# Optimization experiments

Hardware: AMD Instinct MI355X
Metric: run time of the kernel (lower is better)

The kernel has to match this reference:

```python
import jax, jax.numpy as jnp
import numpy as np
from jax import lax

# ---- model dims (match init_kwargs) ----
D = 2048        # hidden_size
HD = 128        # head_dim
HQ = 16         # num_q_heads (= expanded_num_heads)
HK = 8          # num_k_heads = num_v_heads
CONV = 4        # conv_size
CHUNK = 64      # chunk_size
NUM_ITER = 30   # chebyshev iterations
RIDGE = 0.02
EPS = 1e-6


def setup_inputs() -> dict:
    key = jax.random.key(0)
    ks = jax.random.split(key, 20)
    s = 0.02
    inp = {}
    inp['hidden_states'] = jax.random.normal(ks[0], (1, 1024, D), jnp.float32)
    inp['Wq'] = jax.random.normal(ks[1], (D, HQ * HD), jnp.float32) * s
    inp['Wk'] = jax.random.normal(ks[2], (D, HK * HD), jnp.float32) * s
    inp['Wv'] = jax.random.normal(ks[3], (D, HK * HD), jnp.float32) * s
    inp['conv_q'] = jax.random.normal(ks[4], (HQ * HD, CONV), jnp.float32) * 0.3
    inp['conv_k'] = jax.random.normal(ks[5], (HK * HD, CONV), jnp.float32) * 0.3
    inp['conv_v'] = jax.random.normal(ks[6], (HK * HD, CONV), jnp.float32) * 0.3
    inp['Wa'] = jax.random.normal(ks[7], (D, HQ), jnp.float32) * s
    # A_log = log(Uniform(0,16)) as in torch init
    inp['A_log'] = jnp.log(jax.random.uniform(ks[8], (HQ,), jnp.float32, 1e-3, 16.0))
    # dt_bias = inverse-softplus of dt ~ LogUniform(1e-3, 1e-1)
    dt = jnp.exp(jax.random.uniform(ks[9], (HQ,), jnp.float32) * (np.log(0.1) - np.log(0.001)) + np.log(0.001))
    dt = jnp.clip(dt, 1e-4, None)
    inp['dt_bias'] = dt + jnp.log(-jnp.expm1(-dt))
    inp['Wb'] = jax.random.normal(ks[10], (D, HQ), jnp.float32) * s
    inp['bb'] = jnp.zeros((HQ,), jnp.float32)
    inp['Walpha'] = jax.random.normal(ks[11], (D, HQ), jnp.float32) * s
    inp['balpha'] = jnp.zeros((HQ,), jnp.float32)
    inp['Wg'] = jax.random.normal(ks[12], (D, HQ * HD), jnp.float32) * s
    inp['norm_w'] = jnp.ones((HD,), jnp.float32)
    inp['Wo'] = jax.random.normal(ks[13], (HQ * HD, D), jnp.float32) * s
    return inp


def short_conv(x, w):
    # causal depthwise conv1d (kernel=CONV) + silu; x:[B,L,C], w:[C,K]
    K = w.shape[1]
    L = x.shape[1]
    xp = jnp.pad(x, ((0, 0), (K - 1, 0), (0, 0)))
    y = sum(xp[:, j:j + L, :] * w[:, j] for j in range(K))
    return jax.nn.silu(y)


def cheb_solve(A, b, lmin, lmax, num_iter):
    # Chebyshev semi-iteration for SPD A x = b, eigenvalue bounds [lmin, lmax].
    # A, b: [..., d, d]; lmin scalar; lmax: [..., 1, 1]
    theta = (lmax + lmin) / 2.0
    delta = (lmax - lmin) / 2.0
    sigma1 = theta / delta
    x = jnp.zeros_like(b)
    r = b
    rho = 1.0 / sigma1
    dvec = r / theta
    def body(carry, _):
        x, r, dvec, rho = carry
        x = x + dvec
        r = r - jnp.einsum('...de,...ef->...df', A, dvec)
        rho_n = 1.0 / (2.0 * sigma1 - rho)
        dvec = rho_n * rho * dvec + (2.0 * rho_n / delta) * r
        return (x, r, dvec, rho_n), None
    (x, _, _, _), _ = lax.scan(body, (x, r, dvec, rho), None, length=num_iter)
    return x


def reference(hidden_states, Wq, Wk, Wv, conv_q, conv_k, conv_v, Wa, A_log, dt_bias,
              Wb, bb, Walpha, balpha, Wg, norm_w, Wo):
    x = hidden_states
    B, L, _ = x.shape
    H, Hk, d, C = HQ, HK, HD, CHUNK
    Nc = L // C

    # projections + short causal convs with silu
    q = short_conv(x @ Wq, conv_q).reshape(B, L, H, d) * (d ** -0.5)  # gla rescale
    k = short_conv(x @ Wk, conv_k).reshape(B, L, Hk, d)
    v = short_conv(x @ Wv, conv_v).reshape(B, L, Hk, d)
    grp = H // Hk
    k = jnp.repeat(k, grp, axis=2)  # GQA expand: (h g) ordering
    v = jnp.repeat(v, grp, axis=2)

    # gates
    glog = -jnp.exp(A_log) * jax.nn.softplus(x @ Wa + dt_bias)   # [B,L,H], log forgetting gate <= 0
    beta = jax.nn.sigmoid(x @ Wb + bb)                           # [B,L,H]
    alpha = jax.nn.sigmoid(x @ Walpha + balpha)                  # [B,L,H]

    # chunk: [B,H,Nc,C,...]
    def ch(t):
        return t.reshape(B, Nc, C, H, -1).transpose(0, 3, 1, 2, 4)
    qc, kc, vc = ch(q), ch(k), ch(v)
    glc = glog.reshape(B, Nc, C, H).transpose(0, 3, 1, 2)   # [B,H,Nc,C]
    bc = beta.reshape(B, Nc, C, H).transpose(0, 3, 1, 2)

    cs = jnp.cumsum(glc, axis=-1)         # inclusive cumulative log-decay within chunk
    G = cs[..., -1]                        # total chunk decay [B,H,Nc]
    w_end = jnp.exp(G[..., None] - cs) * bc
    dHn = jnp.einsum('bhnc,bhncd,bhnce->bhnde', w_end, kc, kc)  # gram increment (forgetting_gate_kk)
    dBn = jnp.einsum('bhnc,bhncd,bhnce->bhnde', w_end, kc, vc)  # kv increment
    dg = jnp.exp(G)

    # inter-chunk state recurrence (scan over chunks)
    def step(carry, inp):
        Hs, Bs = carry
        g_n, dH_n, dB_n = inp
        out = (Hs, Bs)  # state at chunk START
        Hs = g_n[..., None, None] * Hs + dH_n
        Bs = g_n[..., None, None] * Bs + dB_n
        return (Hs, Bs), out
    init = (jnp.zeros((B, H, d, d), x.dtype), jnp.zeros((B, H, d, d), x.dtype))
    inputs = (dg.transpose(2, 0, 1), dHn.transpose(2, 0, 1, 3, 4), dBn.transpose(2, 0, 1, 3, 4))
    _, (H0, B0) = lax.scan(step, init, inputs)  # [Nc,B,H,d,d]

    # ridge-regularized Kalman solve per chunk via Chebyshev
    A = H0 + RIDGE * jnp.eye(d, dtype=x.dtype)
    lmax = jnp.trace(A, axis1=-2, axis2=-1)[..., None, None]  # trace >= lambda_max for SPD
    X = cheb_solve(A, B0, RIDGE, lmax, NUM_ITER)              # [Nc,B,H,d,d]
    Xc = X.transpose(1, 2, 0, 3, 4)                           # [B,H,Nc,d,d]

    # inter-chunk readout (through solved state)
    o_inter = jnp.exp(cs)[..., None] * jnp.einsum('bhncd,bhnde->bhnce', qc, Xc)
    # intra-chunk causal gated attention
    diff = cs[..., :, None] - cs[..., None, :]                # [B,H,Nc,C,C]
    mask = jnp.tril(jnp.ones((C, C), bool))
    dmat = jnp.exp(jnp.where(mask, diff, -1e30))
    scores = jnp.einsum('bhncd,bhnjd->bhncj', qc, kc) * dmat * bc[..., None, :]
    o_intra = jnp.einsum('bhncj,bhnjd->bhncd', scores, vc)

    o = (o_inter + o_intra).transpose(0, 2, 3, 1, 4).reshape(B, L, H, d)
    o = o + alpha[..., None] * v   # alpha connection (residual value path)

    # gated RMSNorm + output projection
    g_out = (x @ Wg).reshape(B, L, H, d)
    o = o * lax.rsqrt(jnp.mean(o * o, axis=-1, keepdims=True) + EPS) * norm_w
    o = o * jax.nn.silu(g_out)
    return o.reshape(B, L, H * d) @ Wo
```

## Files before the change

### kernel.cpp

```cpp
#include <hip/hip_runtime.h>
#include <math.h>


#define LSEQ 1024
#define DM   2048
#define NHQ  16
#define NHK  8
#define HDIM 128
#define NCH  16
#define CSZ  64

typedef __attribute__((ext_vector_type(8))) short short8;
typedef __attribute__((ext_vector_type(4))) float floatx4;

__device__ __forceinline__ unsigned short f2bf(float f) {
  unsigned int u = __float_as_uint(f);
  u += 0x7fffu + ((u >> 16) & 1u);
  return (unsigned short)(u >> 16);
}
__device__ __forceinline__ float bf2f(unsigned short u) {
  return __uint_as_float(((unsigned int)u) << 16);
}

__device__ __forceinline__ void tcast_fat(
    const float* __restrict__ W, unsigned short* __restrict__ Wt,
    int K, int N, int bn, int bk, int tid, float* __restrict__ t) {
  int k0 = bk * 128, n0 = bn * 64;
#pragma unroll
  for (int i = 0; i < 8; ++i) {
    int u = tid + i * 256;
    int r = u >> 4, c4 = u & 15;
    float4 v = *(const float4*)(W + (size_t)(k0 + r) * N + n0 + c4 * 4);
    float* dst = t + r * 65 + c4 * 4;
    dst[0] = v.x; dst[1] = v.y; dst[2] = v.z; dst[3] = v.w;
  }
  __syncthreads();
#pragma unroll
  for (int i = 0; i < 4; ++i) {
    int u2 = tid + i * 256;
    int klow = u2 & 7, nlow = (u2 >> 3) & 7;
    int khigh = (u2 >> 6) & 1, nhigh = (u2 >> 7) & 7;
    int k8 = (klow + khigh * 8) * 8;
    int nn = nlow + nhigh * 8;
    unsigned short o8[8];
#pragma unroll
    for (int j = 0; j < 8; ++j) o8[j] = f2bf(t[(k8 + j) * 65 + nn]);
    *(uint4*)(Wt + (size_t)(n0 + nn) * K + k0 + k8) = *(uint4*)o8;
  }
}

__global__ __launch_bounds__(256) void prep_kernel(
    const float* __restrict__ x, const float* __restrict__ Wq,
    const float* __restrict__ Wk, const float* __restrict__ Wv,
    const float* __restrict__ Wg, unsigned short* __restrict__ xb16,
    unsigned short* __restrict__ WtAll,
    const float* __restrict__ Wa, const float* __restrict__ Wbeta,
    const float* __restrict__ Wal, const float* __restrict__ A_log,
    const float* __restrict__ dtb, const float* __restrict__ bbv,
    const float* __restrict__ balv, float* __restrict__ glog,
    float* __restrict__ beta, float* __restrict__ alpha) {
  __shared__ float smem[128 * 65];
  int b = blockIdx.x, tid = threadIdx.x;
  if (b < 1024) {
    float* xr = smem;
    float* part = smem + 2048;
    int ts = b;
    for (int i = tid; i < 512; i += 256)
      ((float4*)xr)[i] = ((const float4*)(x + (size_t)ts * 2048))[i];
    __syncthreads();
    int o = tid >> 2, p = tid & 3;
    float s = 0.f;
    if (o < 48) {
      const float* W = (o < 16) ? Wa : (o < 32) ? Wbeta : Wal;
      int h = o & 15;
      int k0 = p * 512;
      for (int k = k0; k < k0 + 512; ++k) s = fmaf(xr[k], W[k * 16 + h], s);
    }
    part[tid] = s;
    __syncthreads();
    if (o < 48 && p == 0) {
      float dot = part[tid] + part[tid + 1] + part[tid + 2] + part[tid + 3];
      int h = o & 15;
      if (o < 16) {
        float za = dot + dtb[h];
        float sp = fmaxf(za, 0.f) + log1pf(expf(-fabsf(za)));
        glog[ts * 16 + h] = -expf(A_log[h]) * sp;
      } else if (o < 32) {
        beta[ts * 16 + h] = 1.f / (1.f + expf(-(dot + bbv[h])));
      } else {
        alpha[ts * 16 + h] = 1.f / (1.f + expf(-(dot + balv[h])));
      }
    }
  } else if (b < 2560) {
    int r = b - 1024;
    if (r < 512) {
      tcast_fat(Wq, WtAll, 2048, 2048, r & 31, r >> 5, tid, smem);
    } else if (r < 768) {
      int q = r - 512;
      tcast_fat(Wk, WtAll + (size_t)2048 * 2048, 2048, 1024, q & 15, q >> 4,
                tid, smem);
    } else if (r < 1024) {
      int q = r - 768;
      tcast_fat(Wv, WtAll + (size_t)3072 * 2048, 2048, 1024, q & 15, q >> 4,
                tid, smem);
    } else {
      int q = r - 1024;
      tcast_fat(Wg, WtAll + (size_t)4096 * 2048, 2048, 2048, q & 31, q >> 5,
                tid, smem);
    }
  } else {
    int i0 = (b - 2560) * 1024 + tid;
#pragma unroll
    for (int i = 0; i < 4; ++i) {
      int idx = i0 + i * 256;
      float4 v = ((const float4*)x)[idx];
      ushort4 u;
      u.x = f2bf(v.x); u.y = f2bf(v.y); u.z = f2bf(v.z); u.w = f2bf(v.w);
      ((ushort4*)xb16)[idx] = u;
    }
  }
}

__global__ __launch_bounds__(256) void gemm_bf16(
    const unsigned short* __restrict__ A, const unsigned short* __restrict__ Bt,
    float* __restrict__ C, int M, int N, int K) {
  __shared__ unsigned short As[128 * 72];
  __shared__ unsigned short Bs[64 * 72];
  int tid = threadIdx.x;
  int wave = tid >> 6, lane = tid & 63;
  int ln = lane & 15, hi = lane >> 4;
  int wm = wave & 1, wn = wave >> 1;
  int m0 = blockIdx.y * 128, n0 = blockIdx.x * 64;

  floatx4 acc[4][2];
#pragma unroll
  for (int mt = 0; mt < 4; ++mt)
#pragma unroll
    for (int nt = 0; nt < 2; ++nt) acc[mt][nt] = (floatx4)(0.f);

  for (int k0 = 0; k0 < K; k0 += 64) {
#pragma unroll
    for (int g = 0; g < 4; ++g) {
      int l = tid + g * 256;
      int m = l >> 3, go = l & 7;
      uint4 v = *(const uint4*)(A + (size_t)(m0 + m) * K + k0 + go * 8);
      *(uint4*)(As + m * 72 + go * 8) = v;
    }
#pragma unroll
    for (int g = 0; g < 2; ++g) {
      int l = tid + g * 256;
      int n = l >> 3, go = l & 7;
      uint4 v = *(const uint4*)(Bt + (size_t)(n0 + n) * K + k0 + go * 8);
      *(uint4*)(Bs + n * 72 + go * 8) = v;
    }
    __syncthreads();
#pragma unroll
    for (int kb = 0; kb < 2; ++kb) {
      short8 a[4], b[2];
#pragma unroll
      for (int mt = 0; mt < 4; ++mt)
        a[mt] = *(const short8*)(As + (wm * 64 + mt * 16 + ln) * 72 + kb * 32 + hi * 8);
#pragma unroll
      for (int nt = 0; nt < 2; ++nt)
        b[nt] = *(const short8*)(Bs + (wn * 32 + nt * 16 + ln) * 72 + kb * 32 + hi * 8);
#pragma unroll
      for (int mt = 0; mt < 4; ++mt)
#pragma unroll
        for (int nt = 0; nt < 2; ++nt)
          acc[mt][nt] = __builtin_amdgcn_mfma_f32_16x16x32_bf16(
              a[mt], b[nt], acc[mt][nt], 0, 0, 0);
    }
    __syncthreads();
  }
#pragma unroll
  for (int mt = 0; mt < 4; ++mt)
#pragma unroll
    for (int nt = 0; nt < 2; ++nt) {
      int col = n0 + wn * 32 + nt * 16 + ln;
      int rowb = m0 + wm * 64 + mt * 16 + hi * 4;
#pragma unroll
      for (int r = 0; r < 4; ++r)
        C[(size_t)(rowb + r) * N + col] = acc[mt][nt][r];
    }
}

__device__ __forceinline__ float conv_core(
    const float* __restrict__ xin, const float* __restrict__ w,
    int idx, int instride, int nch, float scale) {
  int t = idx / nch, ch = idx - t * nch;
  float acc = 0.f;
#pragma unroll
  for (int j = 0; j < 4; ++j) {
    int tt = t + j - 3;
    float xv = (tt >= 0) ? xin[(size_t)tt * instride + ch] : 0.f;
    acc = fmaf(xv, w[ch * 4 + j], acc);
  }
  return acc / (1.f + expf(-acc)) * scale;
}

__global__ __launch_bounds__(256) void conv_all(
    const float* __restrict__ xall, const float* __restrict__ convq,
    const float* __restrict__ convk, const float* __restrict__ convv,
    unsigned short* __restrict__ qs16, float* __restrict__ ks2,
    unsigned short* __restrict__ ks16, float* __restrict__ vs2,
    const float* __restrict__ glog, const float* __restrict__ beta,
    float* __restrict__ cs, float* __restrict__ wend) {
  int b = blockIdx.x, tid = threadIdx.x;
  if (b < 8192) {
    int idx = b * 256 + tid;
    qs16[idx] = f2bf(conv_core(xall, convq, idx, 6144, 2048,
                               0.08838834764831845f));
  } else if (b < 12288) {
    int idx = (b - 8192) * 256 + tid;
    float v = conv_core(xall + 2048, convk, idx, 6144, 1024, 1.0f);
    ks2[idx] = v;
    ks16[idx] = f2bf(v);
  } else if (b < 16384) {
    int idx = (b - 12288) * 256 + tid;
    vs2[idx] = conv_core(xall + 3072, convv, idx, 6144, 1024, 1.0f);
  } else {
    int idx = tid;
    int n = idx & 15;
    float acc = 0.f;
    for (int c = 0; c < CSZ; ++c) {
      acc += glog[(n * CSZ + c) * NHQ + (idx >> 4)];
      cs[idx * CSZ + c] = acc;
    }
    float G = acc;
    for (int c = 0; c < CSZ; ++c) {
      wend[idx * CSZ + c] =
          expf(G - cs[idx * CSZ + c]) * beta[(n * CSZ + c) * NHQ + (idx >> 4)];
    }
  }
}

__global__ __launch_bounds__(256) void dhb_kernel(
    const float* __restrict__ ks, const float* __restrict__ vs,
    const float* __restrict__ wend, float* __restrict__ dH,
    float* __restrict__ dB, unsigned short* __restrict__ vT16) {
  __shared__ uint4 smem4[4096];
  int bid = blockIdx.x;
  int tid = threadIdx.x;

  if (bid >= 256) {
    float* t = (float*)smem4;
    int b = bid - 256;
    size_t gbase = ((size_t)(b >> 3)) * 65536 + ((size_t)(b & 7)) * 128;
#pragma unroll
    for (int g = 0; g < 8; ++g) {
      int i = tid + g * 256;
      int c = i >> 5, e4 = i & 31;
      float4 v = *(const float4*)(vs + gbase + (size_t)c * 1024 + e4 * 4);
      t[c * 132 + e4 * 4 + 0] = v.x;
      t[c * 132 + e4 * 4 + 1] = v.y;
      t[c * 132 + e4 * 4 + 2] = v.z;
      t[c * 132 + e4 * 4 + 3] = v.w;
    }
    __syncthreads();
    int e = tid >> 1, half = tid & 1;
    size_t obase = ((size_t)b << 13) + (size_t)e * 64 + half * 32;
#pragma unroll
    for (int cc = 0; cc < 8; ++cc) {
      int c0 = half * 32 + cc * 4;
      ushort4 u;
      u.x = f2bf(t[(c0 + 0) * 132 + e]);
      u.y = f2bf(t[(c0 + 1) * 132 + e]);
      u.z = f2bf(t[(c0 + 2) * 132 + e]);
      u.w = f2bf(t[(c0 + 3) * 132 + e]);
      *(ushort4*)(vT16 + obase + cc * 4) = u;
    }
    return;
  }

  unsigned short (*skF)[8192] = (unsigned short (*)[8192])smem4;
  unsigned short (*svF)[8192] =
      (unsigned short (*)[8192])((unsigned short*)smem4 + 16384);
  int h = bid >> 4, n = bid & 15;
  int hk = h >> 1;

#pragma unroll
  for (int p = 0; p < 4; ++p) {
    int t2 = tid + p * 256;
    int c0 = (t2 >> 7) << 3;
    int e = t2 & 127;
    int base = ((e >> 4) * 2 + (c0 >> 5)) * 512 +
               ((c0 & 31) >> 3) * 128 + (e & 15) * 8;
    unsigned short kh[8], kl[8], vh[8], vl[8];
#pragma unroll
    for (int j = 0; j < 8; ++j) {
      int c = c0 + j;
      float s = sqrtf(wend[bid * 64 + c]);
      size_t g = (size_t)(n * 64 + c) * 1024 + hk * 128 + e;
      float kf = s * ks[g];
      float vf = s * vs[g];
      unsigned short khh = f2bf(kf);
      kh[j] = khh; kl[j] = f2bf(kf - bf2f(khh));
      unsigned short vhh = f2bf(vf);
      vh[j] = vhh; vl[j] = f2bf(vf - bf2f(vhh));
    }
    *(uint4*)(&skF[0][base]) = *(uint4*)kh;
    *(uint4*)(&skF[1][base]) = *(uint4*)kl;
    *(uint4*)(&svF[0][base]) = *(uint4*)vh;
    *(uint4*)(&svF[1][base]) = *(uint4*)vl;
  }
  __syncthreads();

  int w = tid >> 6, lane = tid & 63;
  int ln = lane & 15, hi = lane >> 4;

  short8 ah[2][2], al[2][2];
#pragma unroll
  for (int mti = 0; mti < 2; ++mti) {
    int mt = w * 2 + mti;
#pragma unroll
    for (int ct = 0; ct < 2; ++ct) {
      ah[mti][ct] = *(const short8*)(&skF[0][((mt * 2 + ct) * 64 + lane) * 8]);
      al[mti][ct] = *(const short8*)(&skF[1][((mt * 2 + ct) * 64 + lane) * 8]);
    }
  }

  size_t gb = (size_t)bid << 14;
#pragma unroll
  for (int which = 0; which < 2; ++which) {
    const unsigned short (*BF)[8192] = which ? svF : skF;
    float* outp = which ? dB : dH;
#pragma unroll
    for (int nt = 0; nt < 8; ++nt) {
      floatx4 a0 = (floatx4)(0.f), a1 = (floatx4)(0.f);
#pragma unroll
      for (int ct = 0; ct < 2; ++ct) {
        short8 bh = *(const short8*)(&BF[0][((nt * 2 + ct) * 64 + lane) * 8]);
        short8 bl = *(const short8*)(&BF[1][((nt * 2 + ct) * 64 + lane) * 8]);
        a0 = __builtin_amdgcn_mfma_f32_16x16x32_bf16(ah[0][ct], bh, a0, 0, 0, 0);
        a0 = __builtin_amdgcn_mfma_f32_16x16x32_bf16(ah[0][ct], bl, a0, 0, 0, 0);
        a0 = __builtin_amdgcn_mfma_f32_16x16x32_bf16(al[0][ct], bh, a0, 0, 0, 0);
        a1 = __builtin_amdgcn_mfma_f32_16x16x32_bf16(ah[1][ct], bh, a1, 0, 0, 0);
        a1 = __builtin_amdgcn_mfma_f32_16x16x32_bf16(ah[1][ct], bl, a1, 0, 0, 0);
        a1 = __builtin_amdgcn_mfma_f32_16x16x32_bf16(al[1][ct], bh, a1, 0, 0, 0);
      }
      int e = nt * 16 + ln;
#pragma unroll
      for (int rg = 0; rg < 4; ++rg) {
        int d0 = (w * 2 + 0) * 16 + hi * 4 + rg;
        int d1 = (w * 2 + 1) * 16 + hi * 4 + rg;
        outp[gb + (size_t)d0 * 128 + e] = a0[rg];
        outp[gb + (size_t)d1 * 128 + e] = a1[rg];
      }
    }
  }
}

__global__ __launch_bounds__(256) void scan_kernel(
    float* __restrict__ dH, float* __restrict__ dB,
    const float* __restrict__ cs) {
  int idx = blockIdx.x * 256 + threadIdx.x;
  int h = idx >> 14, de = idx & 16383;
  float Hs = 0.f, Bs = 0.f;
  bool diag = ((de % 129) == 0);
#pragma unroll 1
  for (int n = 0; n < NCH; ++n) {
    size_t off = ((size_t)(h * 16 + n) << 14) + de;
    float dh = dH[off], db = dB[off];
    dH[off] = diag ? (Hs + 0.02f) : Hs;
    dB[off] = Bs;
    float g = expf(cs[(h * 16 + n) * CSZ + (CSZ - 1)]);
    Hs = fmaf(g, Hs, dh);
    Bs = fmaf(g, Bs, db);
  }
}

__global__ __launch_bounds__(256) void afrag_kernel(
    float* __restrict__ Aall, float* __restrict__ traces) {
  int bid = blockIdx.x;
  float* Ag = Aall + ((size_t)bid << 14);
  __shared__ float As[16384];
  int tid = threadIdx.x;
  for (int i = tid; i < 4096; i += 256)
    ((float4*)As)[i] = ((const float4*)Ag)[i];
  __syncthreads();
  if (tid < 64) {
    float tv = As[tid * 129] + As[(tid + 64) * 129];
#pragma unroll
    for (int off = 32; off; off >>= 1) tv += __shfl_down(tv, off);
    if (tid == 0) traces[bid] = tv;
  }
  unsigned short* Ah = (unsigned short*)Ag;
  unsigned short* Al = Ah + 16384;
#pragma unroll
  for (int c8 = 0; c8 < 8; ++c8) {
    int s0 = tid * 64 + c8 * 8;
    int frag = s0 >> 9, mlane = (s0 >> 3) & 63;
    int m = ((frag >> 2) << 4) + (mlane & 15);
    int k = ((frag & 3) << 5) + ((mlane >> 4) << 3);
    unsigned short hi[8], lo[8];
#pragma unroll
    for (int j = 0; j < 8; ++j) {
      float a = As[m * 128 + k + j];
      unsigned short h = f2bf(a);
      hi[j] = h;
      lo[j] = f2bf(a - bf2f(h));
    }
    *(uint4*)(Ah + s0) = *(uint4*)hi;
    *(uint4*)(Al + s0) = *(uint4*)lo;
  }
}

__global__ __launch_bounds__(256, 4) void cheb_kernel(
    const unsigned short* __restrict__ Afrag, const float* __restrict__ traces,
    float* __restrict__ Ball) {
  int bid = blockIdx.x;
  int bm = bid & 255;
  int cb = bid >> 8;
  const unsigned short* __restrict__ Ah = Afrag + ((size_t)bm << 15);
  float* __restrict__ Bg = Ball + ((size_t)bm << 14);
  __shared__ unsigned short dT[2][2048];
  int tid = threadIdx.x;
  int w = tid >> 6, lane = tid & 63;
  int ln = lane & 15, q = lane >> 4;

  float lmax = traces[bm];
  const float lmin = 0.02f;
  float theta = 0.5f * (lmax + lmin);
  float delta = 0.5f * (lmax - lmin);
  float sigma1 = theta / delta;
  float rho = delta / theta;
  float invtheta = 1.f / theta;

  short8 afr[2][4][2];
#pragma unroll
  for (int mt = 0; mt < 2; ++mt)
#pragma unroll
    for (int kt = 0; kt < 4; ++kt) {
      int f = (w * 2 + mt) * 4 + kt;
      afr[mt][kt][0] = *(const short8*)(Ah + ((f * 64 + lane) << 3));
      afr[mt][kt][1] = *(const short8*)(Ah + 16384 + ((f * 64 + lane) << 3));
    }

  int wrB[2];
#pragma unroll
  for (int mt = 0; mt < 2; ++mt)
    wrB[mt] = w * 512 + (((mt * 2 + (q >> 1)) & 3) * 16 + ln) * 8 +
              ((q & 1) << 2);

  float xx[2][4], rr[2][4], dd[2][4];
#pragma unroll
  for (int mt = 0; mt < 2; ++mt) {
    ushort4 pack;
    unsigned short* pp = (unsigned short*)&pack;
#pragma unroll
    for (int rg = 0; rg < 4; ++rg) {
      float b = Bg[(w * 32 + mt * 16 + q * 4 + rg) * 128 + cb * 16 + ln];
      rr[mt][rg] = b;
      xx[mt][rg] = 0.f;
      unsigned short dq = f2bf(b * invtheta);
      dd[mt][rg] = bf2f(dq);
      pp[rg] = dq;
    }
    *(ushort4*)(&dT[0][wrB[mt]]) = pack;
  }
  __syncthreads();

#pragma unroll 1
  for (int it = 0; it < 30; ++it) {
    const unsigned short* dTr = dT[it & 1];
    unsigned short* dTw = dT[(it & 1) ^ 1];
    floatx4 a0 = (floatx4)(0.f), a1 = (floatx4)(0.f);
#pragma unroll
    for (int kt = 0; kt < 4; ++kt) {
      short8 df = *(const short8*)(dTr + kt * 512 + lane * 8);
      a0 = __builtin_amdgcn_mfma_f32_16x16x32_bf16(afr[0][kt][0], df, a0, 0, 0, 0);
      a0 = __builtin_amdgcn_mfma_f32_16x16x32_bf16(afr[0][kt][1], df, a0, 0, 0, 0);
      a1 = __builtin_amdgcn_mfma_f32_16x16x32_bf16(afr[1][kt][0], df, a1, 0, 0, 0);
      a1 = __builtin_amdgcn_mfma_f32_16x16x32_bf16(afr[1][kt][1], df, a1, 0, 0, 0);
    }
    float rho_n = 1.f / (2.f * sigma1 - rho);
    float c1s = rho_n * rho;
    float c2s = 2.f * rho_n / delta;
#pragma unroll
    for (int mt = 0; mt < 2; ++mt) {
      ushort4 pack;
      unsigned short* pp = (unsigned short*)&pack;
#pragma unroll
      for (int rg = 0; rg < 4; ++rg) {
        xx[mt][rg] += dd[mt][rg];
        rr[mt][rg] -= mt ? a1[rg] : a0[rg];
        float dn = fmaf(c1s, dd[mt][rg], c2s * rr[mt][rg]);
        unsigned short dq = f2bf(dn);
        dd[mt][rg] = bf2f(dq);
        pp[rg] = dq;
      }
      *(ushort4*)(&dTw[wrB[mt]]) = pack;
    }
    rho = rho_n;
    __syncthreads();
  }

  unsigned short* Xf = (unsigned short*)Bg;
#pragma unroll
  for (int mt = 0; mt < 2; ++mt) {
    ushort4 h4, l4;
    unsigned short* hp = (unsigned short*)&h4;
    unsigned short* lp = (unsigned short*)&l4;
#pragma unroll
    for (int rg = 0; rg < 4; ++rg) {
      float xv = xx[mt][rg];
      unsigned short h = f2bf(xv);
      hp[rg] = h;
      lp[rg] = f2bf(xv - bf2f(h));
    }
    int lhi = wrB[mt];
    int llo = lhi + 2048;
    *(ushort4*)(Xf + ((lhi >> 5) << 8) + (cb << 5) + (lhi & 31)) = h4;
    *(ushort4*)(Xf + ((llo >> 5) << 8) + (cb << 5) + (llo & 31)) = l4;
  }
}

__global__ __launch_bounds__(256) void attn_kernel(
    const unsigned short* __restrict__ q16, const unsigned short* __restrict__ k16,
    const unsigned short* __restrict__ vT16, const unsigned short* __restrict__ Xf,
    const float* __restrict__ vs, const float* __restrict__ cs,
    const float* __restrict__ beta, const float* __restrict__ alpha,
    float* __restrict__ o) {
  int bid = blockIdx.x;
  int h = bid >> 4, n = bid & 15;
  int hk = h >> 1;
  __shared__ unsigned short qb[64 * 136];
  __shared__ unsigned short kb[64 * 136];
  __shared__ unsigned short Sb[64 * 72];
  __shared__ float csL[64], ecsL[64], betaL[64], alphaL[64];
  int tid = threadIdx.x;
  int w = tid >> 6, lane = tid & 63;
  int ln = lane & 15, hi = lane >> 4;

  {
    size_t qgb = (((size_t)(n * 64)) * 16 + h) * 128;
    size_t kgb = (((size_t)(n * 64)) * 8 + hk) * 128;
#pragma unroll
    for (int g = 0; g < 4; ++g) {
      int i = tid + g * 256;
      int c = i >> 4, ch = i & 15;
      *(uint4*)(qb + c * 136 + ch * 8) =
          *(const uint4*)(q16 + qgb + (size_t)c * 2048 + ch * 8);
      *(uint4*)(kb + c * 136 + ch * 8) =
          *(const uint4*)(k16 + kgb + (size_t)c * 1024 + ch * 8);
    }
    if (tid < 64) {
      float cv = cs[bid * 64 + tid];
      csL[tid] = cv;
      ecsL[tid] = expf(cv);
      betaL[tid] = beta[(n * 64 + tid) * 16 + h];
      alphaL[tid] = alpha[(n * 64 + tid) * 16 + h];
    }
  }
  __syncthreads();

  short8 aq[4];
#pragma unroll
  for (int dt = 0; dt < 4; ++dt)
    aq[dt] = *(const short8*)(qb + (w * 16 + ln) * 136 + dt * 32 + hi * 8);

  const unsigned short* Xb = Xf + ((size_t)bid << 15);
  floatx4 acc[8];
#pragma unroll
  for (int et = 0; et < 8; ++et) {
    floatx4 a = (floatx4)(0.f);
#pragma unroll
    for (int dt = 0; dt < 4; ++dt) {
      int base = ((dt * 16 + (lane >> 2)) << 8) + (et << 5) + ((lane & 3) << 3);
      short8 xh = *(const short8*)(Xb + base);
      short8 xl = *(const short8*)(Xb + base + 16384);
      a = __builtin_amdgcn_mfma_f32_16x16x32_bf16(aq[dt], xh, a, 0, 0, 0);
      a = __builtin_amdgcn_mfma_f32_16x16x32_bf16(aq[dt], xl, a, 0, 0, 0);
    }
    acc[et] = a;
  }
#pragma unroll
  for (int et = 0; et < 8; ++et)
#pragma unroll
    for (int rg = 0; rg < 4; ++rg)
      acc[et][rg] *= ecsL[w * 16 + hi * 4 + rg];

#pragma unroll
  for (int jt = 0; jt < 4; ++jt) {
    if (jt <= w) {
      floatx4 s = (floatx4)(0.f);
#pragma unroll
      for (int dt = 0; dt < 4; ++dt) {
        short8 bk = *(const short8*)(kb + (jt * 16 + ln) * 136 + dt * 32 + hi * 8);
        s = __builtin_amdgcn_mfma_f32_16x16x32_bf16(aq[dt], bk, s, 0, 0, 0);
      }
      int j = jt * 16 + ln;
      float csj = csL[j], bj = betaL[j];
#pragma unroll
      for (int rg = 0; rg < 4; ++rg) {
        int c = w * 16 + hi * 4 + rg;
        float v = (j <= c) ? s[rg] * expf(csL[c] - csj) * bj : 0.f;
        Sb[c * 72 + j] = f2bf(v);
      }
    } else {
#pragma unroll
      for (int rg = 0; rg < 4; ++rg)
        Sb[(w * 16 + hi * 4 + rg) * 72 + jt * 16 + ln] = 0;
    }
  }

  const unsigned short* vTb = vT16 + ((size_t)(n * 8 + hk) << 13);
#pragma unroll
  for (int et = 0; et < 8; ++et) {
#pragma unroll
    for (int kt = 0; kt < 2; ++kt) {
      short8 as = *(const short8*)(Sb + (w * 16 + ln) * 72 + kt * 32 + hi * 8);
      short8 bv = *(const short8*)(vTb + (et * 16 + ln) * 64 + kt * 32 + hi * 8);
      acc[et] = __builtin_amdgcn_mfma_f32_16x16x32_bf16(as, bv, acc[et], 0, 0, 0);
    }
  }

#pragma unroll
  for (int et = 0; et < 8; ++et) {
#pragma unroll
    for (int rg = 0; rg < 4; ++rg) {
      int c = w * 16 + hi * 4 + rg, e = et * 16 + ln;
      size_t oaddr = (((size_t)(n * 64 + c)) * 16 + h) * 128 + e;
      size_t vaddr = (((size_t)(n * 64 + c)) * 8 + hk) * 128 + e;
      o[oaddr] = acc[et][rg] + alphaL[c] * vs[vaddr];
    }
  }
}

__global__ __launch_bounds__(256) void rmso_kernel(
    const float* __restrict__ o, const float* __restrict__ xall,
    const float* __restrict__ norm_w, unsigned short* __restrict__ onorm,
    const float* __restrict__ Wo, unsigned short* __restrict__ WtWo) {
  __shared__ float t[128 * 65];
  int b = blockIdx.x, tid = threadIdx.x;
  if (b < 512) {
    tcast_fat(Wo, WtWo, 2048, 2048, b & 31, b >> 5, tid, t);
  } else {
    int bb = b - 512;
    int wave = tid >> 6, lane = tid & 63;
    int row = bb * 4 + wave;
    size_t base = (size_t)row * HDIM;
    size_t gbase = (size_t)(row >> 4) * 6144 + 4096 + (size_t)(row & 15) * HDIM;
    float v0 = o[base + lane], v1 = o[base + lane + 64];
    float ss = fmaf(v0, v0, v1 * v1);
#pragma unroll
    for (int off = 32; off; off >>= 1) ss += __shfl_down(ss, off);
    ss = __shfl(ss, 0);
    float rinv = rsqrtf(ss * (1.f / 128.f) + 1e-6f);
    float g0 = xall[gbase + lane], g1 = xall[gbase + lane + 64];
    float s0 = g0 / (1.f + expf(-g0));
    float s1 = g1 / (1.f + expf(-g1));
    onorm[base + lane]      = f2bf(v0 * rinv * norm_w[lane] * s0);
    onorm[base + lane + 64] = f2bf(v1 * rinv * norm_w[lane + 64] * s1);
  }
}

extern "C" void kernel_launch(void* const* d_in, const int* in_sizes, int n_in,
                              void* d_out, int out_size, void* d_ws,
                              size_t ws_size, hipStream_t stream) {
  (void)in_sizes; (void)n_in; (void)out_size; (void)ws_size;
  const float* x      = (const float*)d_in[0];
  const float* Wq     = (const float*)d_in[1];
  const float* Wk     = (const float*)d_in[2];
  const float* Wv     = (const float*)d_in[3];
  const float* convq  = (const float*)d_in[4];
  const float* convk  = (const float*)d_in[5];
  const float* convv  = (const float*)d_in[6];
  const float* Wa     = (const float*)d_in[7];
  const float* A_log  = (const float*)d_in[8];
  const float* dtb    = (const float*)d_in[9];
  const float* Wb     = (const float*)d_in[10];
  const float* bbv    = (const float*)d_in[11];
  const float* Wal    = (const float*)d_in[12];
  const float* balv   = (const float*)d_in[13];
  const float* Wg     = (const float*)d_in[14];
  const float* norm_w = (const float*)d_in[15];
  const float* Wo     = (const float*)d_in[16];
  float* out = (float*)d_out;

  float* p = (float*)d_ws;
  float* xall  = p; p += 6291456;
  float* qslot = p; p += 2097152;
  float* ks2   = p; p += 1048576;
  float* vs2   = p; p += 1048576;
  float* ob    = p; p += 2097152;
  float* glog  = p; p += 16384;
  float* beta  = p; p += 16384;
  float* alpha = p; p += 16384;
  float* csb   = p; p += 16384;
  float* wend  = p; p += 16384;
  float* traces= p; p += 16384;
  float* dHn   = p; p += 4194304;
  float* dBn   = p; p += 4194304;
  unsigned short* xb16 = (unsigned short*)p; p += 1048576;

  unsigned short* qs16 = (unsigned short*)qslot;
  unsigned short* ks16 = qs16 + 2097152;
  unsigned short* vT16 = ks16 + 1048576;
  unsigned short* WtAll = (unsigned short*)dHn;
  unsigned short* WtWo  = (unsigned short*)ks2;
  unsigned short* onorm16 = xb16;

  dim3 blk(256);
  prep_kernel<<<3072, blk, 0, stream>>>(x, Wq, Wk, Wv, Wg, xb16, WtAll,
                                        Wa, Wb, Wal, A_log, dtb, bbv, balv,
                                        glog, beta, alpha);
  gemm_bf16<<<dim3(96, 8), blk, 0, stream>>>(xb16, WtAll, xall, 1024, 6144, 2048);
  conv_all<<<16385, blk, 0, stream>>>(xall, convq, convk, convv,
                                      qs16, ks2, ks16, vs2,
                                      glog, beta, csb, wend);
  dhb_kernel<<<384, blk, 0, stream>>>(ks2, vs2, wend, dHn, dBn, vT16);
  scan_kernel<<<1024, blk, 0, stream>>>(dHn, dBn, csb);
  afrag_kernel<<<256, blk, 0, stream>>>(dHn, traces);
  cheb_kernel<<<2048, blk, 0, stream>>>((unsigned short*)dHn, traces, dBn);
  attn_kernel<<<256, blk, 0, stream>>>(qs16, ks16, vT16, (unsigned short*)dBn,
                                       vs2, csb, beta, alpha, ob);
  rmso_kernel<<<4608, blk, 0, stream>>>(ob, xall, norm_w, onorm16, Wo, WtWo);
  gemm_bf16<<<dim3(32, 8), blk, 0, stream>>>(onorm16, WtWo, out, 1024, 2048, 2048);
}
```

Baseline: 420.4 us.

## Use direct global-to-LDS loads and wider N tile in bf16 GEMM

Replaces register-staged global loads with global_load_lds direct-to-LDS transfers in the GEMM and templatizes the N tile width, using 128 columns for the QKVG projection. This aims to cut VGPR traffic and instruction count in tile loading and to improve reuse of A tiles. LDS padding is removed, because direct loads need contiguous rows, which risks LDS bank conflicts on the fragment reads.

```diff
diff --git a/kernel.cpp b/kernel.cpp
--- a/kernel.cpp
+++ b/kernel.cpp
@@ -20,6 +20,13 @@
 }
 __device__ __forceinline__ float bf2f(unsigned short u) {
   return __uint_as_float(((unsigned int)u) << 16);
+}
+
+__device__ __forceinline__ void gload16(const unsigned short* g,
+                                        unsigned short* l) {
+  __builtin_amdgcn_global_load_lds(
+      (const __attribute__((address_space(1))) unsigned int*)g,
+      (__attribute__((address_space(3))) unsigned int*)l, 16, 0, 0);
 }
 
 __device__ __forceinline__ void tcast_fat(
@@ -121,52 +128,54 @@
   }
 }
 
-__global__ __launch_bounds__(256) void gemm_bf16(
+template <int BN>
+__global__ __launch_bounds__(256) void gemm_lds(
     const unsigned short* __restrict__ A, const unsigned short* __restrict__ Bt,
     float* __restrict__ C, int M, int N, int K) {
-  __shared__ unsigned short As[128 * 72];
-  __shared__ unsigned short Bs[64 * 72];
+  __shared__ unsigned short As[128 * 64];
+  __shared__ unsigned short Bs[BN * 64];
+  constexpr int NT = BN / 32;
+  constexpr int BCH = BN / 32;
   int tid = threadIdx.x;
   int wave = tid >> 6, lane = tid & 63;
   int ln = lane & 15, hi = lane >> 4;
   int wm = wave & 1, wn = wave >> 1;
-  int m0 = blockIdx.y * 128, n0 = blockIdx.x * 64;
-
-  floatx4 acc[4][2];
+  int m0 = blockIdx.y * 128, n0 = blockIdx.x * BN;
+  int lrow = lane >> 3, lcol = (lane & 7) * 8;
+
+  floatx4 acc[4][NT];
 #pragma unroll
   for (int mt = 0; mt < 4; ++mt)
 #pragma unroll
-    for (int nt = 0; nt < 2; ++nt) acc[mt][nt] = (floatx4)(0.f);
+    for (int nt = 0; nt < NT; ++nt) acc[mt][nt] = (floatx4)(0.f);
 
   for (int k0 = 0; k0 < K; k0 += 64) {
 #pragma unroll
-    for (int g = 0; g < 4; ++g) {
-      int l = tid + g * 256;
-      int m = l >> 3, go = l & 7;
-      uint4 v = *(const uint4*)(A + (size_t)(m0 + m) * K + k0 + go * 8);
-      *(uint4*)(As + m * 72 + go * 8) = v;
-    }
-#pragma unroll
-    for (int g = 0; g < 2; ++g) {
-      int l = tid + g * 256;
-      int n = l >> 3, go = l & 7;
-      uint4 v = *(const uint4*)(Bt + (size_t)(n0 + n) * K + k0 + go * 8);
-      *(uint4*)(Bs + n * 72 + go * 8) = v;
+    for (int i = 0; i < 4; ++i) {
+      int c = wave * 4 + i;
+      gload16(A + (size_t)(m0 + c * 8 + lrow) * K + k0 + lcol, As + c * 512);
+    }
+#pragma unroll
+    for (int i = 0; i < BCH; ++i) {
+      int c = wave * BCH + i;
+      gload16(Bt + (size_t)(n0 + c * 8 + lrow) * K + k0 + lcol, Bs + c * 512);
     }
     __syncthreads();
 #pragma unroll
     for (int kb = 0; kb < 2; ++kb) {
-      short8 a[4], b[2];
+      short8 a[4], b[NT];
 #pragma unroll
       for (int mt = 0; mt < 4; ++mt)
-        a[mt] = *(const short8*)(As + (wm * 64 + mt * 16 + ln) * 72 + kb * 32 + hi * 8);
-#pragma unroll
-      for (int nt = 0; nt < 2; ++nt)
-        b[nt] = *(const short8*)(Bs + (wn * 32 + nt * 16 + ln) * 72 + kb * 32 + hi * 8);
+        a[mt] = *(const short8*)(As + (wm * 64 + mt * 16 + ln) * 64 +
+                                 kb * 32 + hi * 8);
+#pragma unroll
+      for (int nt = 0; nt < NT; ++nt)
+        b[nt] = *(const short8*)(Bs + (wn * (BN / 2) + nt * 16 + ln) * 64 +
+                                 kb * 32 + hi * 8);
 #pragma unroll
       for (int mt = 0; mt < 4; ++mt)
 #pragma unroll
-        for (int nt = 0; nt < 2; ++nt)
+        for (int nt = 0; nt < NT; ++nt)
           acc[mt][nt] = __builtin_amdgcn_mfma_f32_16x16x32_bf16(
               a[mt], b[nt], acc[mt][nt], 0, 0, 0);
     }
@@ -175,8 +184,8 @@
 #pragma unroll
   for (int mt = 0; mt < 4; ++mt)
 #pragma unroll
-    for (int nt = 0; nt < 2; ++nt) {
-      int col = n0 + wn * 32 + nt * 16 + ln;
+    for (int nt = 0; nt < NT; ++nt) {
+      int col = n0 + wn * (BN / 2) + nt * 16 + ln;
       int rowb = m0 + wm * 64 + mt * 16 + hi * 4;
 #pragma unroll
       for (int r = 0; r < 4; ++r)
@@ -705,7 +714,8 @@
   prep_kernel<<<3072, blk, 0, stream>>>(x, Wq, Wk, Wv, Wg, xb16, WtAll,
                                         Wa, Wb, Wal, A_log, dtb, bbv, balv,
                                         glog, beta, alpha);
-  gemm_bf16<<<dim3(96, 8), blk, 0, stream>>>(xb16, WtAll, xall, 1024, 6144, 2048);
+  gemm_lds<128><<<dim3(48, 8), blk, 0, stream>>>(xb16, WtAll, xall,
+                                                 1024, 6144, 2048);
   conv_all<<<16385, blk, 0, stream>>>(xall, convq, convk, convv,
                                       qs16, ks2, ks16, vs2,
                                       glog, beta, csb, wend);
@@ -716,5 +726,6 @@
   attn_kernel<<<256, blk, 0, stream>>>(qs16, ks16, vT16, (unsigned short*)dBn,
                                        vs2, csb, beta, alpha, ob);
   rmso_kernel<<<4608, blk, 0, stream>>>(ob, xall, norm_w, onorm16, Wo, WtWo);
-  gemm_bf16<<<dim3(32, 8), blk, 0, stream>>>(onorm16, WtWo, out, 1024, 2048, 2048);
-}
+  gemm_lds<64><<<dim3(32, 8), blk, 0, stream>>>(onorm16, WtWo, out,
+                                                1024, 2048, 2048);
+}
```

Result: slower. 429.4 us (+2.2%).
